# Performance work log

Measured on AMD Instinct MI355X. Metric: run time of the kernel, lower is better.

Reference implementation:

```python
import jax, jax.numpy as jnp
import numpy as np

DIM = 1024
NUM_HEADS = 16
HEAD_DIM = DIM // NUM_HEADS
PHI = (1 + 5 ** 0.5) / 2


def setup_inputs() -> dict:
    key = jax.random.key(0)
    ks = jax.random.split(key, 9)
    s = 1.0 / np.sqrt(DIM)
    x = jax.random.normal(ks[0], (1, 4096, DIM), dtype=jnp.float32)
    Wq = jax.random.uniform(ks[1], (DIM, DIM), jnp.float32, -s, s)
    bq = jax.random.uniform(ks[2], (DIM,), jnp.float32, -s, s)
    Wk = jax.random.uniform(ks[3], (DIM, DIM), jnp.float32, -s, s)
    bk = jax.random.uniform(ks[4], (DIM,), jnp.float32, -s, s)
    Wv = jax.random.uniform(ks[5], (DIM, DIM), jnp.float32, -s, s)
    bv = jax.random.uniform(ks[6], (DIM,), jnp.float32, -s, s)
    Wo = jax.random.uniform(ks[7], (DIM, DIM), jnp.float32, -s, s)
    bo = jax.random.uniform(ks[8], (DIM,), jnp.float32, -s, s)
    return {"x": x, "Wq": Wq, "bq": bq, "Wk": Wk, "bk": bk,
            "Wv": Wv, "bv": bv, "Wo": Wo, "bo": bo}


def reference(x, Wq, bq, Wk, bk, Wv, bv, Wo, bo):
    B, S, _ = x.shape
    H, D = NUM_HEADS, HEAD_DIM
    scale = D ** (-0.5)
    # projections, reshape to [B, H, S, D]
    q = (x @ Wq.T + bq).reshape(B, S, H, D).transpose(0, 2, 1, 3)
    k = (x @ Wk.T + bk).reshape(B, S, H, D).transpose(0, 2, 1, 3)
    v = (x @ Wv.T + bv).reshape(B, S, H, D).transpose(0, 2, 1, 3)
    attn = jnp.einsum('bhqd,bhkd->bhqk', q, k) * scale
    attn = jax.nn.softmax(attn, axis=-1)
    # fractal per-head scalar modulation: phi^{-i} for head i
    scales = PHI ** (-jnp.arange(H, dtype=jnp.float32))
    attn = attn * scales[None, :, None, None]
    out = jnp.einsum('bhqk,bhkd->bhqd', attn, v)
    out = out.transpose(0, 2, 1, 3).reshape(B, S, H * D)
    return out @ Wo.T + bo
```

## Files before the change

kernel.cpp:

```cpp
#include <hip/hip_runtime.h>


typedef unsigned short u16;
typedef unsigned int u32;
typedef __attribute__((ext_vector_type(8))) short short8;
typedef __attribute__((ext_vector_type(4))) float f32x4;
typedef __attribute__((ext_vector_type(4))) u16 u16x4;
typedef __attribute__((ext_vector_type(4))) u32 u32x4;

#define KDIM 1024
#define QSCALE 0.18033688011112042f
#define LOG2PHI 0.6942419136306174f

__device__ __forceinline__ u16 f2bf(float f) {
  u32 u = __builtin_bit_cast(u32, f);
  u32 r = (u + 0x7fffu + ((u >> 16) & 1u)) >> 16;
  return (u16)r;
}

__device__ __forceinline__ u32 cvtpk(float lo, float hi) {
  u32 r;
  asm("v_cvt_pk_bf16_f32 %0, %1, %2" : "=v"(r) : "v"(lo), "v"(hi));
  return r;
}

#define EXP2(x) __builtin_amdgcn_exp2f(x)

__device__ __forceinline__ f32x4 fzero() {
  f32x4 z; z[0] = 0.f; z[1] = 0.f; z[2] = 0.f; z[3] = 0.f; return z;
}

__global__ __launch_bounds__(256) void cvt_all(
    const float* __restrict__ x, const float* __restrict__ wq,
    const float* __restrict__ wk, const float* __restrict__ wv,
    const float* __restrict__ wo, u16* __restrict__ xb,
    u16* __restrict__ wqkv, u16* __restrict__ wob) {
  const int i = blockIdx.x * 256 + threadIdx.x;
  const float* src;
  u16* dst;
  int off;
  if (i < 1048576) { src = x; dst = xb; off = i; }
  else if (i < 1310720) { src = wq; dst = wqkv; off = i - 1048576; }
  else if (i < 1572864) { src = wk; dst = wqkv + 1048576; off = i - 1310720; }
  else if (i < 1835008) { src = wv; dst = wqkv + 2097152; off = i - 1572864; }
  else { src = wo; dst = wob; off = i - 1835008; }
  f32x4 v = *(const f32x4*)(src + (size_t)off * 4);
  u16x4 o;
  o[0] = f2bf(v[0]); o[1] = f2bf(v[1]); o[2] = f2bf(v[2]); o[3] = f2bf(v[3]);
  *(u16x4*)(dst + (size_t)off * 4) = o;
}

template <int MODE>
__global__ __launch_bounds__(256) void gemm_bt(
    const u16* __restrict__ A, const u16* __restrict__ Bw,
    const float* __restrict__ bias0, const float* __restrict__ bias1,
    const float* __restrict__ bias2,
    u16* __restrict__ qo, u16* __restrict__ ko, u16* __restrict__ vto,
    float* __restrict__ co) {
  __shared__ u16 As[128 * 64];
  __shared__ u16 Bs[128 * 64];
  const int tid = threadIdx.x;
  const int w = tid >> 6, lane = tid & 63;
  const int wr = w >> 1, wc = w & 1;
  const int bm = blockIdx.x, bn = blockIdx.y;
  const int lr = lane & 15, lg = lane >> 4;
  const int srow8 = lane >> 3;
  const int schunk = lane & 7;

  f32x4 acc[4][4];
#pragma unroll
  for (int m = 0; m < 4; ++m)
#pragma unroll
    for (int n = 0; n < 4; ++n) acc[m][n] = fzero();

  for (int kt = 0; kt < KDIM / 64; ++kt) {
#pragma unroll
    for (int it = 0; it < 4; ++it) {
      const int rowt = (w * 4 + it) * 8 + srow8;
      const int ck = schunk ^ (rowt & 7);
      const u16* sa = A + (size_t)(bm * 128 + rowt) * KDIM + kt * 64 + ck * 8;
      const u16* sb = Bw + (size_t)(bn * 128 + rowt) * KDIM + kt * 64 + ck * 8;
      auto ga = (const __attribute__((address_space(1))) u32*)sa;
      auto la = (__attribute__((address_space(3))) u32*)&As[(w * 4 + it) * 512];
      __builtin_amdgcn_global_load_lds(ga, la, 16, 0, 0);
      auto gb = (const __attribute__((address_space(1))) u32*)sb;
      auto lb = (__attribute__((address_space(3))) u32*)&Bs[(w * 4 + it) * 512];
      __builtin_amdgcn_global_load_lds(gb, lb, 16, 0, 0);
    }
    __syncthreads();
#pragma unroll
    for (int kk = 0; kk < 2; ++kk) {
      short8 af[4], bf[4];
#pragma unroll
      for (int m = 0; m < 4; ++m) {
        const int row = wr * 64 + m * 16 + lr;
        const int kb = kk * 64 + lg * 16;
        af[m] = *(const short8*)((const char*)As + row * 128 + (kb ^ ((row & 7) << 4)));
      }
#pragma unroll
      for (int n = 0; n < 4; ++n) {
        const int row = wc * 64 + n * 16 + lr;
        const int kb = kk * 64 + lg * 16;
        bf[n] = *(const short8*)((const char*)Bs + row * 128 + (kb ^ ((row & 7) << 4)));
      }
#pragma unroll
      for (int m = 0; m < 4; ++m)
#pragma unroll
        for (int n = 0; n < 4; ++n)
          acc[m][n] = __builtin_amdgcn_mfma_f32_16x16x32_bf16(af[m], bf[n], acc[m][n], 0, 0, 0);
    }
    __syncthreads();
  }

#pragma unroll
  for (int m = 0; m < 4; ++m) {
#pragma unroll
    for (int n = 0; n < 4; ++n) {
#pragma unroll
      for (int r = 0; r < 4; ++r) {
        const int srow = bm * 128 + wr * 64 + m * 16 + lg * 4 + r;
        const int col = bn * 128 + wc * 64 + n * 16 + lr;
        float v = acc[m][n][r];
        if (MODE == 0) {
          const int which = col >> 10;
          const int hd = col & 1023;
          const int h = hd >> 6, d = hd & 63;
          const float* bp = (which == 0) ? bias0 : (which == 1) ? bias1 : bias2;
          v += bp[hd];
          if (which == 0) {
            qo[(size_t)h * 262144 + (size_t)srow * 64 + d] = f2bf(v * QSCALE);
          } else if (which == 1) {
            ko[(size_t)h * 262144 + (size_t)srow * 64 + d] = f2bf(v);
          } else {
            const int kb5 = ((srow >> 2) & 3) * 8 + ((srow >> 4) & 1) * 4 + (srow & 3);
            const int lane2 = (kb5 >> 3) * 16 + (d & 15);
            vto[((size_t)h * 128 + (srow >> 5)) * 2048 + (d >> 4) * 512 +
                lane2 * 8 + (kb5 & 7)] = f2bf(v);
          }
        } else {
          co[(size_t)srow * 1024 + col] = v + bias0[col];
        }
      }
    }
  }
}

__global__ __launch_bounds__(256) void attn_kernel(const u16* __restrict__ Q,
                                                   const u16* __restrict__ K,
                                                   const u16* __restrict__ VT,
                                                   u16* __restrict__ O) {
  __shared__ u16 Ks[2][2][4096];
  __shared__ float cL[128];
  const int tid = threadIdx.x;
  const int w = tid >> 6, lane = tid & 63;
  const int qsub = w >> 1, kh = w & 1;
  const int bid = blockIdx.x;
  const int id2 = (bid & 7) * 64 + (bid >> 3);
  const int h = id2 >> 5, qt = id2 & 31;
  const int lr = lane & 15, lg = lane >> 4;
  const int qrow0 = qt * 128 + qsub * 64;

  const u16* kg = K + (size_t)h * 262144;
  const u16* vg = VT + (size_t)h * 262144;

  short8 qf[4][2];
#pragma unroll
  for (int qg = 0; qg < 4; ++qg)
#pragma unroll
    for (int dg = 0; dg < 2; ++dg)
      qf[qg][dg] = *(const short8*)(Q + (size_t)h * 262144 +
                                    (size_t)(qrow0 + qg * 16 + lr) * 64 + dg * 32 + lg * 8);

#define STAGE1(KH, B, J)                                                      \
  do {                                                                        \
    _Pragma("unroll")                                                         \
    for (int it = 0; it < 2; ++it) {                                          \
      const int c = it * 256 + tid;                                           \
      const int row = c >> 3;                                                 \
      const int sc = (c & 7) ^ (row & 7);                                     \
      const u16* gk = kg + (size_t)((J) + row) * 64 + sc * 8;                 \
      __builtin_amdgcn_global_load_lds(                                       \
          (const __attribute__((address_space(1))) u32*)gk,                   \
          (__attribute__((address_space(3))) u32*)&Ks[KH][B][c * 8], 16, 0, 0); \
    }                                                                         \
  } while (0)
#define STAGE(B, T) do { STAGE1(0, B, (T) * 64); STAGE1(1, B, 2048 + (T) * 64); } while (0)

  f32x4 o[4][4];
#pragma unroll
  for (int dg = 0; dg < 4; ++dg)
#pragma unroll
    for (int qg = 0; qg < 4; ++qg) o[dg][qg] = fzero();
  float lsum[4] = {0.f, 0.f, 0.f, 0.f};

  STAGE(0, 0);
  __syncthreads();

  int b = 0;
  for (int t = 0; t < 32; ++t) {
    if (t < 31) STAGE(b ^ 1, t + 1);
    const u16* vbase = vg + (size_t)(kh * 64 + t * 2) * 2048 + lane * 8;
    short8 vf[8];
#pragma unroll
    for (int i = 0; i < 8; ++i) vf[i] = *(const short8*)(vbase + i * 512);

    u32x4 pb[2][4];
#pragma unroll
    for (int half = 0; half < 2; ++half) {
      f32x4 s[2][4];
#pragma unroll
      for (int ki = 0; ki < 2; ++ki) {
        const int row = (half * 2 + ki) * 16 + lr;
        const int sw = (row & 7) << 4;
        const char* base = (const char*)&Ks[kh][b][0] + row * 128;
        const short8 k0 = *(const short8*)(base + ((lg * 16) ^ sw));
        const short8 k1 = *(const short8*)(base + ((64 + lg * 16) ^ sw));
#pragma unroll
        for (int qg = 0; qg < 4; ++qg) {
          s[ki][qg] = __builtin_amdgcn_mfma_f32_16x16x32_bf16(k0, qf[qg][0], fzero(), 0, 0, 0);
          s[ki][qg] = __builtin_amdgcn_mfma_f32_16x16x32_bf16(k1, qf[qg][1], s[ki][qg], 0, 0, 0);
        }
      }
#pragma unroll
      for (int qg = 0; qg < 4; ++qg) {
        float rs = 0.f;
#pragma unroll
        for (int ki = 0; ki < 2; ++ki)
#pragma unroll
          for (int r = 0; r < 4; ++r) {
            const float e = EXP2(s[ki][qg][r]);
            s[ki][qg][r] = e;
            rs += e;
          }
        lsum[qg] += rs;
        pb[half][qg][0] = cvtpk(s[0][qg][0], s[0][qg][1]);
        pb[half][qg][1] = cvtpk(s[0][qg][2], s[0][qg][3]);
        pb[half][qg][2] = cvtpk(s[1][qg][0], s[1][qg][1]);
        pb[half][qg][3] = cvtpk(s[1][qg][2], s[1][qg][3]);
      }
    }
#pragma unroll
    for (int dg = 0; dg < 4; ++dg) {
#pragma unroll
      for (int qg = 0; qg < 4; ++qg) {
        o[dg][qg] = __builtin_amdgcn_mfma_f32_16x16x32_bf16(
            vf[dg], __builtin_bit_cast(short8, pb[0][qg]), o[dg][qg], 0, 0, 0);
        o[dg][qg] = __builtin_amdgcn_mfma_f32_16x16x32_bf16(
            vf[4 + dg], __builtin_bit_cast(short8, pb[1][qg]), o[dg][qg], 0, 0, 0);
      }
    }
    __syncthreads();
    b ^= 1;
  }
#undef STAGE
#undef STAGE1

#pragma unroll
  for (int qg = 0; qg < 4; ++qg) {
    lsum[qg] += __shfl_xor(lsum[qg], 16, 64);
    lsum[qg] += __shfl_xor(lsum[qg], 32, 64);
  }

  float* cO = (float*)&Ks[0][0][0];
  if (kh == 1) {
#pragma unroll
    for (int qg = 0; qg < 4; ++qg) {
#pragma unroll
      for (int dg = 0; dg < 4; ++dg)
        *(f32x4*)(cO + qsub * 4096 + (qg * 4 + dg) * 256 + lane * 4) = o[dg][qg];
      cL[qsub * 64 + qg * 16 + lr] = lsum[qg];
    }
  }
  __syncthreads();
  if (kh == 0) {
    const float hs = EXP2(-(float)h * LOG2PHI);
#pragma unroll
    for (int qg = 0; qg < 4; ++qg) {
      const float l = fmaxf(lsum[qg] + cL[qsub * 64 + qg * 16 + lr], 1e-10f);
      const float sc = hs / l;
#pragma unroll
      for (int dg = 0; dg < 4; ++dg) {
        const f32x4 oth = *(const f32x4*)(cO + qsub * 4096 + (qg * 4 + dg) * 256 + lane * 4);
        u16x4 pk;
#pragma unroll
        for (int r = 0; r < 4; ++r) pk[r] = f2bf((o[dg][qg][r] + oth[r]) * sc);
        *(u16x4*)(O + (size_t)(qrow0 + qg * 16 + lr) * 1024 + h * 64 + dg * 16 + lg * 4) = pk;
      }
    }
  }
}

extern "C" void kernel_launch(void* const* d_in, const int* in_sizes, int n_in,
                              void* d_out, int out_size, void* d_ws, size_t ws_size,
                              hipStream_t stream) {
  const float* x = (const float*)d_in[0];
  const float* Wq = (const float*)d_in[1];
  const float* bq = (const float*)d_in[2];
  const float* Wk = (const float*)d_in[3];
  const float* bk = (const float*)d_in[4];
  const float* Wv = (const float*)d_in[5];
  const float* bv = (const float*)d_in[6];
  const float* Wo = (const float*)d_in[7];
  const float* bo = (const float*)d_in[8];
  float* out = (float*)d_out;

  u16* xb = (u16*)d_ws;
  u16* wqkv = xb + 4194304;
  u16* wob = wqkv + 3145728;
  u16* qs = wob + 1048576;
  u16* ks = qs + 4194304;
  u16* vt = ks + 4194304;
  u16* ob = xb;

  cvt_all<<<8192, 256, 0, stream>>>(x, Wq, Wk, Wv, Wo, xb, wqkv, wob);

  gemm_bt<0><<<dim3(32, 24), 256, 0, stream>>>(xb, wqkv, bq, bk, bv, qs, ks, vt, nullptr);
  attn_kernel<<<512, 256, 0, stream>>>(qs, ks, vt, ob);
  gemm_bt<1><<<dim3(32, 8), 256, 0, stream>>>(ob, wob, bo, nullptr, nullptr,
                                              nullptr, nullptr, nullptr, out);
}
```

Measured before the change: 184.3 us.

## Stage V tiles through LDS with async loads alongside K

```diff
diff --git a/kernel.cpp b/kernel.cpp
--- a/kernel.cpp
+++ b/kernel.cpp
@@ -132,10 +132,9 @@
           } else if (which == 1) {
             ko[(size_t)h * 262144 + (size_t)srow * 64 + d] = f2bf(v);
           } else {
-            const int kb5 = ((srow >> 2) & 3) * 8 + ((srow >> 4) & 1) * 4 + (srow & 3);
-            const int lane2 = (kb5 >> 3) * 16 + (d & 15);
-            vto[((size_t)h * 128 + (srow >> 5)) * 2048 + (d >> 4) * 512 +
-                lane2 * 8 + (kb5 & 7)] = f2bf(v);
+            const int k5 = srow & 31;
+            const int kap = ((k5 >> 2) & 3) * 8 + ((k5 >> 4) & 1) * 4 + (k5 & 3);
+            vto[(size_t)h * 262144 + (size_t)d * 4096 + (srow & ~31) + kap] = f2bf(v);
           }
         } else {
           co[(size_t)srow * 1024 + col] = v + bias0[col];
@@ -150,7 +149,7 @@
                                                    const u16* __restrict__ VT,
                                                    u16* __restrict__ O) {
   __shared__ u16 Ks[2][2][4096];
-  __shared__ float cL[128];
+  __shared__ u16 Vs[2][2][4096];
   const int tid = threadIdx.x;
   const int w = tid >> 6, lane = tid & 63;
   const int qsub = w >> 1, kh = w & 1;
@@ -182,6 +181,10 @@
       __builtin_amdgcn_global_load_lds(                                       \
           (const __attribute__((address_space(1))) u32*)gk,                   \
           (__attribute__((address_space(3))) u32*)&Ks[KH][B][c * 8], 16, 0, 0); \
+      const u16* gv = vg + (size_t)row * 4096 + (J) + sc * 8;                 \
+      __builtin_amdgcn_global_load_lds(                                       \
+          (const __attribute__((address_space(1))) u32*)gv,                   \
+          (__attribute__((address_space(3))) u32*)&Vs[KH][B][c * 8], 16, 0, 0); \
     }                                                                         \
   } while (0)
 #define STAGE(B, T) do { STAGE1(0, B, (T) * 64); STAGE1(1, B, 2048 + (T) * 64); } while (0)
@@ -199,56 +202,65 @@
   int b = 0;
   for (int t = 0; t < 32; ++t) {
     if (t < 31) STAGE(b ^ 1, t + 1);
-    const u16* vbase = vg + (size_t)(kh * 64 + t * 2) * 2048 + lane * 8;
+    f32x4 s[4][4];
+    __builtin_amdgcn_s_setprio(1);
+#pragma unroll
+    for (int kg2 = 0; kg2 < 4; ++kg2) {
+      const int row = kg2 * 16 + lr;
+      const int sw = (row & 7) << 4;
+      const char* base = (const char*)&Ks[kh][b][0] + row * 128;
+      const short8 k0 = *(const short8*)(base + ((lg * 16) ^ sw));
+      const short8 k1 = *(const short8*)(base + ((64 + lg * 16) ^ sw));
+#pragma unroll
+      for (int qg = 0; qg < 4; ++qg) {
+        s[kg2][qg] = __builtin_amdgcn_mfma_f32_16x16x32_bf16(k0, qf[qg][0], fzero(), 0, 0, 0);
+        s[kg2][qg] = __builtin_amdgcn_mfma_f32_16x16x32_bf16(k1, qf[qg][1], s[kg2][qg], 0, 0, 0);
+      }
+    }
+    __builtin_amdgcn_s_setprio(0);
     short8 vf[8];
 #pragma unroll
-    for (int i = 0; i < 8; ++i) vf[i] = *(const short8*)(vbase + i * 512);
-
+    for (int dg = 0; dg < 4; ++dg) {
+      const int row = dg * 16 + lr;
+      const int sw = (row & 7) << 4;
+      const char* base = (const char*)&Vs[kh][b][0] + row * 128;
+      vf[dg * 2] = *(const short8*)(base + ((lg * 16) ^ sw));
+      vf[dg * 2 + 1] = *(const short8*)(base + ((64 + lg * 16) ^ sw));
+    }
     u32x4 pb[2][4];
 #pragma unroll
-    for (int half = 0; half < 2; ++half) {
-      f32x4 s[2][4];
-#pragma unroll
-      for (int ki = 0; ki < 2; ++ki) {
-        const int row = (half * 2 + ki) * 16 + lr;
-        const int sw = (row & 7) << 4;
-        const char* base = (const char*)&Ks[kh][b][0] + row * 128;
-        const short8 k0 = *(const short8*)(base + ((lg * 16) ^ sw));
-        const short8 k1 = *(const short8*)(base + ((64 + lg * 16) ^ sw));
-#pragma unroll
-        for (int qg = 0; qg < 4; ++qg) {
-          s[ki][qg] = __builtin_amdgcn_mfma_f32_16x16x32_bf16(k0, qf[qg][0], fzero(), 0, 0, 0);
-          s[ki][qg] = __builtin_amdgcn_mfma_f32_16x16x32_bf16(k1, qf[qg][1], s[ki][qg], 0, 0, 0);
+    for (int qg = 0; qg < 4; ++qg) {
+      float rs = 0.f;
+#pragma unroll
+      for (int kg2 = 0; kg2 < 4; ++kg2)
+#pragma unroll
+        for (int r = 0; r < 4; ++r) {
+          const float e = EXP2(s[kg2][qg][r]);
+          s[kg2][qg][r] = e;
+          rs += e;
         }
-      }
-#pragma unroll
-      for (int qg = 0; qg < 4; ++qg) {
-        float rs = 0.f;
-#pragma unroll
-        for (int ki = 0; ki < 2; ++ki)
-#pragma unroll
-          for (int r = 0; r < 4; ++r) {
-            const float e = EXP2(s[ki][qg][r]);
-            s[ki][qg][r] = e;
-            rs += e;
-          }
-        lsum[qg] += rs;
-        pb[half][qg][0] = cvtpk(s[0][qg][0], s[0][qg][1]);
-        pb[half][qg][1] = cvtpk(s[0][qg][2], s[0][qg][3]);
-        pb[half][qg][2] = cvtpk(s[1][qg][0], s[1][qg][1]);
-        pb[half][qg][3] = cvtpk(s[1][qg][2], s[1][qg][3]);
-      }
-    }
+      lsum[qg] += rs;
+      pb[0][qg][0] = cvtpk(s[0][qg][0], s[0][qg][1]);
+      pb[0][qg][1] = cvtpk(s[0][qg][2], s[0][qg][3]);
+      pb[0][qg][2] = cvtpk(s[1][qg][0], s[1][qg][1]);
+      pb[0][qg][3] = cvtpk(s[1][qg][2], s[1][qg][3]);
+      pb[1][qg][0] = cvtpk(s[2][qg][0], s[2][qg][1]);
+      pb[1][qg][1] = cvtpk(s[2][qg][2], s[2][qg][3]);
+      pb[1][qg][2] = cvtpk(s[3][qg][0], s[3][qg][1]);
+      pb[1][qg][3] = cvtpk(s[3][qg][2], s[3][qg][3]);
+    }
+    __builtin_amdgcn_s_setprio(1);
 #pragma unroll
     for (int dg = 0; dg < 4; ++dg) {
 #pragma unroll
       for (int qg = 0; qg < 4; ++qg) {
         o[dg][qg] = __builtin_amdgcn_mfma_f32_16x16x32_bf16(
-            vf[dg], __builtin_bit_cast(short8, pb[0][qg]), o[dg][qg], 0, 0, 0);
+            vf[dg * 2], __builtin_bit_cast(short8, pb[0][qg]), o[dg][qg], 0, 0, 0);
         o[dg][qg] = __builtin_amdgcn_mfma_f32_16x16x32_bf16(
-            vf[4 + dg], __builtin_bit_cast(short8, pb[1][qg]), o[dg][qg], 0, 0, 0);
-      }
-    }
+            vf[dg * 2 + 1], __builtin_bit_cast(short8, pb[1][qg]), o[dg][qg], 0, 0, 0);
+      }
+    }
+    __builtin_amdgcn_s_setprio(0);
     __syncthreads();
     b ^= 1;
   }
@@ -262,6 +274,7 @@
   }
 
   float* cO = (float*)&Ks[0][0][0];
+  float* cL = (float*)&Vs[0][0][0];
   if (kh == 1) {
 #pragma unroll
     for (int qg = 0; qg < 4; ++qg) {
```

Measured after the change: 198.2 us. 1.08x slower.

## Stage V tiles through LDS with async loads and add MFMA priority hints

Applied to the files above, without the earlier changes.

```diff
diff --git a/kernel.cpp b/kernel.cpp
--- a/kernel.cpp
+++ b/kernel.cpp
@@ -132,10 +132,9 @@
           } else if (which == 1) {
             ko[(size_t)h * 262144 + (size_t)srow * 64 + d] = f2bf(v);
           } else {
-            const int kb5 = ((srow >> 2) & 3) * 8 + ((srow >> 4) & 1) * 4 + (srow & 3);
-            const int lane2 = (kb5 >> 3) * 16 + (d & 15);
-            vto[((size_t)h * 128 + (srow >> 5)) * 2048 + (d >> 4) * 512 +
-                lane2 * 8 + (kb5 & 7)] = f2bf(v);
+            const int k5 = srow & 31;
+            const int kap = ((k5 >> 2) & 3) * 8 + ((k5 >> 4) & 1) * 4 + (k5 & 3);
+            vto[(size_t)h * 262144 + (size_t)d * 4096 + (srow & ~31) + kap] = f2bf(v);
           }
         } else {
           co[(size_t)srow * 1024 + col] = v + bias0[col];
@@ -150,7 +149,7 @@
                                                    const u16* __restrict__ VT,
                                                    u16* __restrict__ O) {
   __shared__ u16 Ks[2][2][4096];
-  __shared__ float cL[128];
+  __shared__ u16 Vs[2][2][4096];
   const int tid = threadIdx.x;
   const int w = tid >> 6, lane = tid & 63;
   const int qsub = w >> 1, kh = w & 1;
@@ -182,6 +181,10 @@
       __builtin_amdgcn_global_load_lds(                                       \
           (const __attribute__((address_space(1))) u32*)gk,                   \
           (__attribute__((address_space(3))) u32*)&Ks[KH][B][c * 8], 16, 0, 0); \
+      const u16* gv = vg + (size_t)row * 4096 + (J) + sc * 8;                 \
+      __builtin_amdgcn_global_load_lds(                                       \
+          (const __attribute__((address_space(1))) u32*)gv,                   \
+          (__attribute__((address_space(3))) u32*)&Vs[KH][B][c * 8], 16, 0, 0); \
     }                                                                         \
   } while (0)
 #define STAGE(B, T) do { STAGE1(0, B, (T) * 64); STAGE1(1, B, 2048 + (T) * 64); } while (0)
@@ -199,15 +202,11 @@
   int b = 0;
   for (int t = 0; t < 32; ++t) {
     if (t < 31) STAGE(b ^ 1, t + 1);
-    const u16* vbase = vg + (size_t)(kh * 64 + t * 2) * 2048 + lane * 8;
-    short8 vf[8];
-#pragma unroll
-    for (int i = 0; i < 8; ++i) vf[i] = *(const short8*)(vbase + i * 512);
-
     u32x4 pb[2][4];
 #pragma unroll
     for (int half = 0; half < 2; ++half) {
       f32x4 s[2][4];
+      __builtin_amdgcn_s_setprio(1);
 #pragma unroll
       for (int ki = 0; ki < 2; ++ki) {
         const int row = (half * 2 + ki) * 16 + lr;
@@ -221,6 +220,7 @@
           s[ki][qg] = __builtin_amdgcn_mfma_f32_16x16x32_bf16(k1, qf[qg][1], s[ki][qg], 0, 0, 0);
         }
       }
+      __builtin_amdgcn_s_setprio(0);
 #pragma unroll
       for (int qg = 0; qg < 4; ++qg) {
         float rs = 0.f;
@@ -239,16 +239,23 @@
         pb[half][qg][3] = cvtpk(s[1][qg][2], s[1][qg][3]);
       }
     }
+    __builtin_amdgcn_s_setprio(1);
 #pragma unroll
     for (int dg = 0; dg < 4; ++dg) {
+      const int row = dg * 16 + lr;
+      const int sw = (row & 7) << 4;
+      const char* base = (const char*)&Vs[kh][b][0] + row * 128;
+      const short8 v0 = *(const short8*)(base + ((lg * 16) ^ sw));
+      const short8 v1 = *(const short8*)(base + ((64 + lg * 16) ^ sw));
 #pragma unroll
       for (int qg = 0; qg < 4; ++qg) {
         o[dg][qg] = __builtin_amdgcn_mfma_f32_16x16x32_bf16(
-            vf[dg], __builtin_bit_cast(short8, pb[0][qg]), o[dg][qg], 0, 0, 0);
+            v0, __builtin_bit_cast(short8, pb[0][qg]), o[dg][qg], 0, 0, 0);
         o[dg][qg] = __builtin_amdgcn_mfma_f32_16x16x32_bf16(
-            vf[4 + dg], __builtin_bit_cast(short8, pb[1][qg]), o[dg][qg], 0, 0, 0);
-      }
-    }
+            v1, __builtin_bit_cast(short8, pb[1][qg]), o[dg][qg], 0, 0, 0);
+      }
+    }
+    __builtin_amdgcn_s_setprio(0);
     __syncthreads();
     b ^= 1;
   }
@@ -262,6 +269,7 @@
   }
 
   float* cO = (float*)&Ks[0][0][0];
+  float* cL = (float*)&Vs[0][0][0];
   if (kh == 1) {
 #pragma unroll
     for (int qg = 0; qg < 4; ++qg) {
```

Result: faster. 160.0 us (-13.2%).
